# Performance work log

Measured on AMD Instinct MI355X. Metric: run time of the kernel, lower is better.

Reference implementation:

```python
import jax, jax.numpy as jnp
import numpy as np

K = 9          # neighbors (module default k=9, dilation=1 -> plain top-k)
COUT = 256     # out_channels
BN_EPS = 1e-5


def setup_inputs() -> dict:
    key = jax.random.key(0)
    k1, k2 = jax.random.split(key, 2)
    x = jax.random.normal(k1, (8, 128, 2048, 1), jnp.float32)          # [B,C,N,1]
    W = jax.random.normal(k2, (COUT, 2 * 128), jnp.float32) * 0.05     # 1x1 conv weight [Cout, 2C]
    gamma = jnp.ones((COUT,), jnp.float32)                             # BN affine scale
    beta = jnp.zeros((COUT,), jnp.float32)                             # BN affine shift
    return {"x": x, "W": W, "gamma": gamma, "beta": beta}


def reference(x, W, gamma, beta):
    # x: [B, C, N, 1] channels-first point features
    xt = jnp.transpose(x[..., 0], (0, 2, 1))                           # [B, N, C]
    B, N, C = xt.shape

    # --- dense KNN graph (matrix form): squared euclidean distance, k nearest ---
    sq = jnp.sum(xt * xt, axis=-1)                                     # [B, N]
    dist = sq[:, :, None] - 2.0 * jnp.einsum('bnc,bmc->bnm', xt, xt) + sq[:, None, :]
    _, nn_idx = jax.lax.top_k(-dist, K)                                # [B, N, K] neighbor indices

    # --- EdgeConv gather: x_i = center, x_j = neighbor ---
    x_j = jax.vmap(lambda f, i: f[i])(xt, nn_idx)                      # [B, N, K, C]
    x_i = xt[:, :, None, :]                                            # [B, N, 1, C]
    feat = jnp.concatenate(
        [jnp.broadcast_to(x_i, (B, N, K, C)), x_j - x_i], axis=-1)     # [B, N, K, 2C]

    # --- 1x1 conv (no bias) as GEMM over channel dim ---
    h = jnp.einsum('bnkc,oc->bnko', feat, W)                           # [B, N, K, Cout]

    # --- BatchNorm2d (training-mode batch stats over B,N,K per channel) ---
    mean = jnp.mean(h, axis=(0, 1, 2))
    var = jnp.var(h, axis=(0, 1, 2))
    hn = (h - mean) * jax.lax.rsqrt(var + BN_EPS) * gamma + beta

    # --- ReLU then max over k neighbors ---
    out = jnp.max(jax.nn.relu(hn), axis=2)                             # [B, N, Cout]
    return jnp.transpose(out, (0, 2, 1))                               # [B, Cout, N]
```

## Files before the change

### kernel.cpp

```cpp
#include <hip/hip_runtime.h>
#include <float.h>
#include <math.h>

#define BATCH 8
#define CHN   128
#define NPTS  2048
#define KNN   9
#define NOUT  256
#define TOTCNT (BATCH*NPTS*KNN)

typedef __attribute__((ext_vector_type(8))) short short8;
typedef __attribute__((ext_vector_type(4))) float f32x4;

__device__ __forceinline__ unsigned short f2bf(float f) {
    unsigned int u = __float_as_uint(f);
    unsigned int r = (u + 0x7FFFu + ((u >> 16) & 1u)) >> 16;
    return (unsigned short)r;
}
__device__ __forceinline__ float bf2f(unsigned short h) {
    return __uint_as_float(((unsigned int)h) << 16);
}

__global__ __launch_bounds__(256) void prep_kernel(const float* __restrict__ x,
                                                   unsigned short* __restrict__ xhi,
                                                   unsigned short* __restrict__ xlo,
                                                   float* __restrict__ sqh) {
    __shared__ float xt[128 * 65];
    __shared__ float psq[256];
    const int b = blockIdx.x, n0 = blockIdx.y * 64, tid = threadIdx.x;
#pragma unroll 4
    for (int p = 0; p < 32; ++p) {
        int c = p * 4 + (tid >> 6), n = tid & 63;
        xt[c * 65 + n] = x[((size_t)b * CHN + c) * NPTS + n0 + n];
    }
    __syncthreads();
    const int n = tid >> 2, cq = tid & 3;
    size_t row = (size_t)(b * NPTS + n0 + n) * CHN;
    float s = 0.f;
#pragma unroll 8
    for (int j = 0; j < 32; ++j) {
        int c = cq * 32 + j;
        float f = xt[c * 65 + n];
        unsigned short h = f2bf(f);
        float hf = bf2f(h);
        unsigned short l = f2bf(f - hf);
        xhi[row + c] = h;
        xlo[row + c] = l;
        s += f * f;
    }
    psq[tid] = s;
    __syncthreads();
    if (tid < 64)
        sqh[b * NPTS + n0 + tid] =
            0.5f * (psq[tid*4] + psq[tid*4+1] + psq[tid*4+2] + psq[tid*4+3]);
}

__global__ __launch_bounds__(256) void wprep_kernel(const float* __restrict__ W,
                                                    unsigned short* __restrict__ whi,
                                                    unsigned short* __restrict__ wlo) {
    int t = blockIdx.x * 256 + threadIdx.x;
    int r = t >> 5, c0 = (t & 31) * 4;
#pragma unroll
    for (int e = 0; e < 4; ++e) {
        int c = c0 + e;
        float v = (r < 256) ? (W[r * 256 + c] - W[r * 256 + 128 + c])
                            : W[(r - 256) * 256 + 128 + c];
        unsigned short h = f2bf(v);
        float hf = bf2f(h);
        unsigned short l = f2bf(v - hf);
        whi[r * 128 + c] = h;
        wlo[r * 128 + c] = l;
    }
}

__global__ __launch_bounds__(256) void knn_mfma(const unsigned short* __restrict__ xhi,
                                                const unsigned short* __restrict__ xlo,
                                                const float* __restrict__ sqh,
                                                float* __restrict__ pd,
                                                int* __restrict__ pi) {
    __shared__ __align__(16) float dts[64 * 132];

    const int tid = threadIdx.x;
    const int b = blockIdx.x, q0 = blockIdx.y * 64, ms = blockIdx.z;
    const int msbase = ms * 512;
    const int wv = tid >> 6, lane = tid & 63;
    const int quad = lane >> 4, col = lane & 15;
    const int koff = quad * 8;
    const int mcol0 = wv * 32;
    const size_t xb = (size_t)b * NPTS * CHN;

    float dl[KNN]; int il[KNN];
#pragma unroll
    for (int k = 0; k < KNN; ++k) { dl[k] = FLT_MAX; il[k] = 0; }

    const int qsc = tid >> 2, ss = tid & 3;
    const int cb = ss * 32;

    auto ins = [&](float v, int idx) {
        if (v < dl[KNN - 1]) {
            bool c0b = v < dl[0];
#pragma unroll
            for (int k = KNN - 1; k >= 1; --k) {
                bool sh   = v < dl[k - 1];
                bool here = v < dl[k];
                float nd = sh ? dl[k - 1] : (here ? v : dl[k]);
                int   ni = sh ? il[k - 1] : (here ? idx : il[k]);
                dl[k] = nd; il[k] = ni;
            }
            if (c0b) { dl[0] = v; il[0] = idx; }
        }
    };

    for (int iter = 0; iter < 4; ++iter) {
        const int mbase = msbase + iter * 128;
        float sm[2];
#pragma unroll
        for (int j = 0; j < 2; ++j)
            sm[j] = sqh[b * NPTS + mbase + mcol0 + j * 16 + col];

        f32x4 acc[4][2];
#pragma unroll
        for (int i = 0; i < 4; ++i)
#pragma unroll
            for (int j = 0; j < 2; ++j) acc[i][j] = (f32x4)0.f;

        for (int chk = 0; chk < 4; ++chk) {
            short8 ah[4], al[4];
#pragma unroll
            for (int i = 0; i < 4; ++i) {
                size_t g = xb + (size_t)(q0 + i * 16 + col) * CHN + chk * 32 + koff;
                ah[i] = *(const short8*)&xhi[g];
                al[i] = *(const short8*)&xlo[g];
            }
#pragma unroll
            for (int j = 0; j < 2; ++j) {
                size_t g = xb + (size_t)(mbase + mcol0 + j * 16 + col) * CHN + chk * 32 + koff;
                short8 bh = *(const short8*)&xhi[g];
                short8 bl = *(const short8*)&xlo[g];
#pragma unroll
                for (int i = 0; i < 4; ++i) {
                    acc[i][j] = __builtin_amdgcn_mfma_f32_16x16x32_bf16(ah[i], bh, acc[i][j], 0, 0, 0);
                    acc[i][j] = __builtin_amdgcn_mfma_f32_16x16x32_bf16(ah[i], bl, acc[i][j], 0, 0, 0);
                    acc[i][j] = __builtin_amdgcn_mfma_f32_16x16x32_bf16(al[i], bh, acc[i][j], 0, 0, 0);
                }
            }
        }

        __syncthreads();
#pragma unroll
        for (int j = 0; j < 2; ++j)
#pragma unroll
            for (int i = 0; i < 4; ++i)
#pragma unroll
                for (int r = 0; r < 4; ++r) {
                    int q_ = i * 16 + quad * 4 + r;
                    dts[q_ * 132 + mcol0 + j * 16 + col] = sm[j] - acc[i][j][r];
                }
        __syncthreads();
        const int ibase = mbase + cb;
#pragma unroll
        for (int jj = 0; jj < 8; ++jj) {
            float4 v = *(const float4*)&dts[qsc * 132 + cb + jj * 4];
            float mn4 = fminf(fminf(v.x, v.y), fminf(v.z, v.w));
            if (mn4 < dl[KNN - 1]) {
                int ib = ibase + jj * 4;
                ins(v.x, ib); ins(v.y, ib + 1); ins(v.z, ib + 2); ins(v.w, ib + 3);
            }
        }
    }

    __syncthreads();
    float* md = dts;
    int*   mi = (int*)(dts + 2304);
#pragma unroll
    for (int k = 0; k < KNN; ++k) {
        md[qsc * 36 + ss * 9 + k] = dl[k];
        mi[qsc * 36 + ss * 9 + k] = il[k];
    }
    __syncthreads();
    if (tid < 64) {
        int base = tid * 36;
        int p0 = 0, p1 = 0, p2 = 0, p3 = 0;
        size_t ob = ((size_t)(b * NPTS + q0 + tid) * 4 + ms) * KNN;
        for (int k = 0; k < KNN; ++k) {
            float v0 = (p0 < KNN) ? md[base + p0]      : FLT_MAX;
            float v1 = (p1 < KNN) ? md[base + 9 + p1]  : FLT_MAX;
            float v2 = (p2 < KNN) ? md[base + 18 + p2] : FLT_MAX;
            float v3 = (p3 < KNN) ? md[base + 27 + p3] : FLT_MAX;
            float best = v0; int sel = 0;
            if (v1 < best) { best = v1; sel = 1; }
            if (v2 < best) { best = v2; sel = 2; }
            if (v3 < best) { best = v3; sel = 3; }
            int idx;
            if      (sel == 0) { idx = mi[base + p0];      p0++; }
            else if (sel == 1) { idx = mi[base + 9 + p1];  p1++; }
            else if (sel == 2) { idx = mi[base + 18 + p2]; p2++; }
            else               { idx = mi[base + 27 + p3]; p3++; }
            pd[ob + k] = best;
            pi[ob + k] = idx;
        }
    }
}

__global__ __launch_bounds__(256) void pq_mfma(const unsigned short* __restrict__ xhi,
                                               const unsigned short* __restrict__ xlo,
                                               const unsigned short* __restrict__ whi,
                                               const unsigned short* __restrict__ wlo,
                                               float* __restrict__ p,
                                               float* __restrict__ q) {
    const int tid = threadIdx.x;
    const int b = blockIdx.x, nt = blockIdx.y, ot = blockIdx.z;
    const int wv = tid >> 6, lane = tid & 63;
    const int quad = lane >> 4, col = lane & 15;
    const int koff = quad * 8;
    const size_t xb = (size_t)b * NPTS * CHN;
    const int nbase = nt * 256 + wv * 64;
    const int obase = ot * 64;

    f32x4 acc[4][4];
#pragma unroll
    for (int i = 0; i < 4; ++i)
#pragma unroll
        for (int j = 0; j < 4; ++j) acc[i][j] = (f32x4)0.f;

    for (int chk = 0; chk < 4; ++chk) {
        short8 ah[4], al[4];
#pragma unroll
        for (int i = 0; i < 4; ++i) {
            size_t g = xb + (size_t)(nbase + i * 16 + col) * CHN + chk * 32 + koff;
            ah[i] = *(const short8*)&xhi[g];
            al[i] = *(const short8*)&xlo[g];
        }
#pragma unroll
        for (int j = 0; j < 4; ++j) {
            size_t g = (size_t)(obase + j * 16 + col) * CHN + chk * 32 + koff;
            short8 bh = *(const short8*)&whi[g];
            short8 bl = *(const short8*)&wlo[g];
#pragma unroll
            for (int i = 0; i < 4; ++i) {
                acc[i][j] = __builtin_amdgcn_mfma_f32_16x16x32_bf16(ah[i], bh, acc[i][j], 0, 0, 0);
                acc[i][j] = __builtin_amdgcn_mfma_f32_16x16x32_bf16(ah[i], bl, acc[i][j], 0, 0, 0);
                acc[i][j] = __builtin_amdgcn_mfma_f32_16x16x32_bf16(al[i], bh, acc[i][j], 0, 0, 0);
            }
        }
    }
    float* dst = (ot < 4) ? p : q;
#pragma unroll
    for (int i = 0; i < 4; ++i)
#pragma unroll
        for (int j = 0; j < 4; ++j) {
            int oc = (obase + j * 16 + col) & 255;
#pragma unroll
            for (int r = 0; r < 4; ++r) {
                int n = nbase + i * 16 + quad * 4 + r;
                dst[(size_t)(b * NPTS + n) * NOUT + oc] = acc[i][j][r];
            }
        }
}

__global__ __launch_bounds__(256) void stats2_kernel(float* __restrict__ p,
                                                     const float* __restrict__ q,
                                                     const float* __restrict__ pd,
                                                     const int* __restrict__ pi,
                                                     float* __restrict__ stats,
                                                     float* __restrict__ hmn) {
    __shared__ int idx_s[32 * KNN];
    const int b = blockIdx.x, n0 = blockIdx.y * 32;
    const int o = threadIdx.x;
    if (threadIdx.x < 32) {
        size_t g = (size_t)(b * NPTS + n0 + threadIdx.x) * 36;
        const float* d = pd + g;
        const int*   i = pi + g;
        int p0 = 0, p1 = 0, p2 = 0, p3 = 0;
#pragma unroll
        for (int k = 0; k < KNN; ++k) {
            float v0 = (p0 < KNN) ? d[p0]      : FLT_MAX;
            float v1 = (p1 < KNN) ? d[9 + p1]  : FLT_MAX;
            float v2 = (p2 < KNN) ? d[18 + p2] : FLT_MAX;
            float v3 = (p3 < KNN) ? d[27 + p3] : FLT_MAX;
            float best = v0; int sel = 0;
            if (v1 < best) { best = v1; sel = 1; }
            if (v2 < best) { best = v2; sel = 2; }
            if (v3 < best) { best = v3; sel = 3; }
            int idx;
            if      (sel == 0) { idx = i[p0];      p0++; }
            else if (sel == 1) { idx = i[9 + p1];  p1++; }
            else if (sel == 2) { idx = i[18 + p2]; p2++; }
            else               { idx = i[27 + p3]; p3++; }
            idx_s[threadIdx.x * KNN + k] = idx;
        }
    }
    __syncthreads();
    const float* qb = q + (size_t)b * NPTS * NOUT + o;
    float s = 0.f, ss = 0.f;
    for (int qq = 0; qq < 32; ++qq) {
        size_t off = (size_t)(b * NPTS + n0 + qq) * NOUT + o;
        float pv = p[off];
        float h[KNN];
#pragma unroll
        for (int k = 0; k < KNN; ++k)
            h[k] = pv + qb[(size_t)idx_s[qq * KNN + k] * NOUT];
        float mx = h[0], mn = h[0];
#pragma unroll
        for (int k = 0; k < KNN; ++k) {
            s += h[k]; ss += h[k] * h[k];
            mx = fmaxf(mx, h[k]); mn = fminf(mn, h[k]);
        }
        p[off] = mx;
        hmn[off] = mn;
    }
    atomicAdd(&stats[o], s);
    atomicAdd(&stats[NOUT + o], ss);
}

__global__ __launch_bounds__(256) void final_kernel(const float* __restrict__ hmx,
                                                    const float* __restrict__ hmn,
                                                    const float* __restrict__ stats,
                                                    const float* __restrict__ gamma,
                                                    const float* __restrict__ beta,
                                                    float* __restrict__ out) {
    __shared__ float tr[256 * 17];
    const int b = blockIdx.x, n0 = blockIdx.y * 16;
    const int o = threadIdx.x;
    const float inv = 1.f / (float)TOTCNT;
    float mean = stats[o] * inv;
    float var  = stats[NOUT + o] * inv - mean * mean;
    float g    = gamma[o] / sqrtf(var + 1e-5f);
    float bet  = beta[o];
    const float* src = (g >= 0.f) ? hmx : hmn;
    for (int qq = 0; qq < 16; ++qq) {
        size_t off = (size_t)(b * NPTS + n0 + qq) * NOUT + o;
        float hn = (src[off] - mean) * g + bet;
        tr[o * 17 + qq] = fmaxf(hn, 0.f);
    }
    __syncthreads();
    int oo = threadIdx.x >> 4, qq = threadIdx.x & 15;
    for (int pass = 0; pass < 16; ++pass) {
        int o_ = pass * 16 + oo;
        out[((size_t)b * NOUT + o_) * NPTS + n0 + qq] = tr[o_ * 17 + qq];
    }
}

extern "C" void kernel_launch(void* const* d_in, const int* in_sizes, int n_in,
                              void* d_out, int out_size, void* d_ws, size_t ws_size,
                              hipStream_t stream) {
    (void)in_sizes; (void)n_in; (void)out_size; (void)ws_size;
    const float* x     = (const float*)d_in[0];
    const float* W     = (const float*)d_in[1];
    const float* gamma = (const float*)d_in[2];
    const float* beta  = (const float*)d_in[3];
    float* out = (float*)d_out;

    char* ws = (char*)d_ws;
    float*          p     = (float*)ws;
    float*          q     = (float*)(ws + (16u << 20));
    unsigned short* xhi   = (unsigned short*)(ws + (32u << 20));
    unsigned short* xlo   = (unsigned short*)(ws + (36u << 20));
    unsigned short* whi   = (unsigned short*)(ws + (40u << 20));
    unsigned short* wlo   = (unsigned short*)(ws + (40u << 20) + 131072);
    float*          hmn   = (float*)(ws + (32u << 20));
    float*          pd    = (float*)(ws + (48u << 20));
    int*            pi    = (int*)  (ws + (51u << 20));
    float*          sqh   = (float*)(ws + (54u << 20));
    float*          stats = (float*)(ws + (54u << 20) + 65536);

    hipMemsetAsync(stats, 0, 2 * NOUT * sizeof(float), stream);
    wprep_kernel <<<64,             256, 0, stream>>>(W, whi, wlo);
    prep_kernel  <<<dim3(8, 32),    256, 0, stream>>>(x, xhi, xlo, sqh);
    knn_mfma     <<<dim3(8, 32, 4), 256, 0, stream>>>(xhi, xlo, sqh, pd, pi);
    pq_mfma      <<<dim3(8, 8, 8),  256, 0, stream>>>(xhi, xlo, whi, wlo, p, q);
    stats2_kernel<<<dim3(8, 64),    256, 0, stream>>>(p, q, pd, pi, stats, hmn);
    final_kernel <<<dim3(8, 128),   256, 0, stream>>>(p, hmn, stats, gamma, beta, out);
}
```

Before: 220.5 us.

## Fuse stats and BN-final via cooperative grid sync, store q and min/max as bf16

Folds the weight-prep kernel into prep_kernel as an extra block row. It also merges the gather/stats and normalize/output kernels into one cooperative kernel. Per-point max/min stay in shared memory across a grid-wide sync, so they are no longer written to and re-read from global memory. The q projection and the max/min values are stored as bf16 to halve gather traffic. This trades away some precision, and the cooperative launch requires all 512 blocks to be co-resident.

```diff
diff --git a/kernel.cpp b/kernel.cpp
--- a/kernel.cpp
+++ b/kernel.cpp
@@ -1,6 +1,9 @@
 #include <hip/hip_runtime.h>
+#include <hip/hip_cooperative_groups.h>
 #include <float.h>
 #include <math.h>
+
+namespace cg = cooperative_groups;
 
 #define BATCH 8
 #define CHN   128
@@ -22,12 +25,30 @@
 }
 
 __global__ __launch_bounds__(256) void prep_kernel(const float* __restrict__ x,
+                                                   const float* __restrict__ W,
                                                    unsigned short* __restrict__ xhi,
                                                    unsigned short* __restrict__ xlo,
+                                                   unsigned short* __restrict__ whi,
+                                                   unsigned short* __restrict__ wlo,
                                                    float* __restrict__ sqh) {
     __shared__ float xt[128 * 65];
     __shared__ float psq[256];
-    const int b = blockIdx.x, n0 = blockIdx.y * 64, tid = threadIdx.x;
+    const int b = blockIdx.x, tid = threadIdx.x;
+    if (blockIdx.y == 32) {
+#pragma unroll
+        for (int e = 0; e < 32; ++e) {
+            int idx = e * 256 + tid;
+            int r = b * 64 + (idx >> 7), c = idx & 127;
+            float v = (r < 256) ? (W[r * 256 + c] - W[r * 256 + 128 + c])
+                                : W[(r - 256) * 256 + 128 + c];
+            unsigned short h = f2bf(v);
+            float hf = bf2f(h);
+            whi[r * 128 + c] = h;
+            wlo[r * 128 + c] = f2bf(v - hf);
+        }
+        return;
+    }
+    const int n0 = blockIdx.y * 64;
 #pragma unroll 4
     for (int p = 0; p < 32; ++p) {
         int c = p * 4 + (tid >> 6), n = tid & 63;
@@ -53,24 +74,6 @@
     if (tid < 64)
         sqh[b * NPTS + n0 + tid] =
             0.5f * (psq[tid*4] + psq[tid*4+1] + psq[tid*4+2] + psq[tid*4+3]);
-}
-
-__global__ __launch_bounds__(256) void wprep_kernel(const float* __restrict__ W,
-                                                    unsigned short* __restrict__ whi,
-                                                    unsigned short* __restrict__ wlo) {
-    int t = blockIdx.x * 256 + threadIdx.x;
-    int r = t >> 5, c0 = (t & 31) * 4;
-#pragma unroll
-    for (int e = 0; e < 4; ++e) {
-        int c = c0 + e;
-        float v = (r < 256) ? (W[r * 256 + c] - W[r * 256 + 128 + c])
-                            : W[(r - 256) * 256 + 128 + c];
-        unsigned short h = f2bf(v);
-        float hf = bf2f(h);
-        unsigned short l = f2bf(v - hf);
-        whi[r * 128 + c] = h;
-        wlo[r * 128 + c] = l;
-    }
 }
 
 __global__ __launch_bounds__(256) void knn_mfma(const unsigned short* __restrict__ xhi,
@@ -207,7 +210,7 @@
                                                const unsigned short* __restrict__ whi,
                                                const unsigned short* __restrict__ wlo,
                                                float* __restrict__ p,
-                                               float* __restrict__ q) {
+                                               unsigned short* __restrict__ q) {
     const int tid = threadIdx.x;
     const int b = blockIdx.x, nt = blockIdx.y, ot = blockIdx.z;
     const int wv = tid >> 6, lane = tid & 63;
@@ -244,7 +247,6 @@
             }
         }
     }
-    float* dst = (ot < 4) ? p : q;
 #pragma unroll
     for (int i = 0; i < 4; ++i)
 #pragma unroll
@@ -253,20 +255,28 @@
 #pragma unroll
             for (int r = 0; r < 4; ++r) {
                 int n = nbase + i * 16 + quad * 4 + r;
-                dst[(size_t)(b * NPTS + n) * NOUT + oc] = acc[i][j][r];
-            }
-        }
-}
-
-__global__ __launch_bounds__(256) void stats2_kernel(float* __restrict__ p,
-                                                     const float* __restrict__ q,
-                                                     const float* __restrict__ pd,
-                                                     const int* __restrict__ pi,
-                                                     float* __restrict__ stats,
-                                                     float* __restrict__ hmn) {
-    __shared__ int idx_s[32 * KNN];
+                size_t off = (size_t)(b * NPTS + n) * NOUT + oc;
+                if (ot < 4) p[off] = acc[i][j][r];
+                else        q[off] = f2bf(acc[i][j][r]);
+            }
+        }
+}
+
+__global__ __launch_bounds__(256) void fused_bn_kernel(const float* __restrict__ p,
+                                                       const unsigned short* __restrict__ qb,
+                                                       const float* __restrict__ pd,
+                                                       const int* __restrict__ pi,
+                                                       float* __restrict__ stats,
+                                                       const float* __restrict__ gamma,
+                                                       const float* __restrict__ beta,
+                                                       float* __restrict__ out) {
+    __shared__ unsigned short hmx_s[32 * 258];
+    __shared__ unsigned short hmn_s[32 * 258];
+    __shared__ int   idx_s[32 * KNN];
+    __shared__ float g_s[256], bet_s[256], mean_s[256];
     const int b = blockIdx.x, n0 = blockIdx.y * 32;
     const int o = threadIdx.x;
+
     if (threadIdx.x < 32) {
         size_t g = (size_t)(b * NPTS + n0 + threadIdx.x) * 36;
         const float* d = pd + g;
@@ -291,53 +301,45 @@
         }
     }
     __syncthreads();
-    const float* qb = q + (size_t)b * NPTS * NOUT + o;
+
+    const unsigned short* qbb = qb + (size_t)b * NPTS * NOUT + o;
     float s = 0.f, ss = 0.f;
     for (int qq = 0; qq < 32; ++qq) {
         size_t off = (size_t)(b * NPTS + n0 + qq) * NOUT + o;
         float pv = p[off];
-        float h[KNN];
-#pragma unroll
-        for (int k = 0; k < KNN; ++k)
-            h[k] = pv + qb[(size_t)idx_s[qq * KNN + k] * NOUT];
-        float mx = h[0], mn = h[0];
+        float mx = -FLT_MAX, mn = FLT_MAX;
 #pragma unroll
         for (int k = 0; k < KNN; ++k) {
-            s += h[k]; ss += h[k] * h[k];
-            mx = fmaxf(mx, h[k]); mn = fminf(mn, h[k]);
-        }
-        p[off] = mx;
-        hmn[off] = mn;
+            float h = pv + bf2f(qbb[(size_t)idx_s[qq * KNN + k] * NOUT]);
+            s += h; ss += h * h;
+            mx = fmaxf(mx, h); mn = fminf(mn, h);
+        }
+        hmx_s[qq * 258 + o] = f2bf(mx);
+        hmn_s[qq * 258 + o] = f2bf(mn);
     }
     atomicAdd(&stats[o], s);
     atomicAdd(&stats[NOUT + o], ss);
-}
-
-__global__ __launch_bounds__(256) void final_kernel(const float* __restrict__ hmx,
-                                                    const float* __restrict__ hmn,
-                                                    const float* __restrict__ stats,
-                                                    const float* __restrict__ gamma,
-                                                    const float* __restrict__ beta,
-                                                    float* __restrict__ out) {
-    __shared__ float tr[256 * 17];
-    const int b = blockIdx.x, n0 = blockIdx.y * 16;
-    const int o = threadIdx.x;
-    const float inv = 1.f / (float)TOTCNT;
-    float mean = stats[o] * inv;
-    float var  = stats[NOUT + o] * inv - mean * mean;
-    float g    = gamma[o] / sqrtf(var + 1e-5f);
-    float bet  = beta[o];
-    const float* src = (g >= 0.f) ? hmx : hmn;
-    for (int qq = 0; qq < 16; ++qq) {
-        size_t off = (size_t)(b * NPTS + n0 + qq) * NOUT + o;
-        float hn = (src[off] - mean) * g + bet;
-        tr[o * 17 + qq] = fmaxf(hn, 0.f);
-    }
-    __syncthreads();
-    int oo = threadIdx.x >> 4, qq = threadIdx.x & 15;
-    for (int pass = 0; pass < 16; ++pass) {
-        int o_ = pass * 16 + oo;
-        out[((size_t)b * NOUT + o_) * NPTS + n0 + qq] = tr[o_ * 17 + qq];
+    __threadfence();
+    cg::this_grid().sync();
+
+    {
+        const float inv = 1.f / (float)TOTCNT;
+        float mean = stats[o] * inv;
+        float var  = stats[NOUT + o] * inv - mean * mean;
+        g_s[o]    = gamma[o] / sqrtf(var + 1e-5f);
+        bet_s[o]  = beta[o];
+        mean_s[o] = mean;
+    }
+    __syncthreads();
+
+    const int qq2 = threadIdx.x & 31, og = threadIdx.x >> 5;
+#pragma unroll 4
+    for (int pass = 0; pass < 32; ++pass) {
+        int o_ = pass * 8 + og;
+        float g = g_s[o_];
+        float v = bf2f((g >= 0.f) ? hmx_s[qq2 * 258 + o_] : hmn_s[qq2 * 258 + o_]);
+        float hn = (v - mean_s[o_]) * g + bet_s[o_];
+        out[((size_t)b * NOUT + o_) * NPTS + n0 + qq2] = fmaxf(hn, 0.f);
     }
 }
 
@@ -353,22 +355,23 @@
 
     char* ws = (char*)d_ws;
     float*          p     = (float*)ws;
-    float*          q     = (float*)(ws + (16u << 20));
+    unsigned short* q     = (unsigned short*)(ws + (16u << 20));
     unsigned short* xhi   = (unsigned short*)(ws + (32u << 20));
     unsigned short* xlo   = (unsigned short*)(ws + (36u << 20));
     unsigned short* whi   = (unsigned short*)(ws + (40u << 20));
     unsigned short* wlo   = (unsigned short*)(ws + (40u << 20) + 131072);
-    float*          hmn   = (float*)(ws + (32u << 20));
     float*          pd    = (float*)(ws + (48u << 20));
     int*            pi    = (int*)  (ws + (51u << 20));
     float*          sqh   = (float*)(ws + (54u << 20));
     float*          stats = (float*)(ws + (54u << 20) + 65536);
 
     hipMemsetAsync(stats, 0, 2 * NOUT * sizeof(float), stream);
-    wprep_kernel <<<64,             256, 0, stream>>>(W, whi, wlo);
-    prep_kernel  <<<dim3(8, 32),    256, 0, stream>>>(x, xhi, xlo, sqh);
-    knn_mfma     <<<dim3(8, 32, 4), 256, 0, stream>>>(xhi, xlo, sqh, pd, pi);
-    pq_mfma      <<<dim3(8, 8, 8),  256, 0, stream>>>(xhi, xlo, whi, wlo, p, q);
-    stats2_kernel<<<dim3(8, 64),    256, 0, stream>>>(p, q, pd, pi, stats, hmn);
-    final_kernel <<<dim3(8, 128),   256, 0, stream>>>(p, hmn, stats, gamma, beta, out);
-}
+    prep_kernel<<<dim3(8, 33),    256, 0, stream>>>(x, W, xhi, xlo, whi, wlo, sqh);
+    knn_mfma   <<<dim3(8, 32, 4), 256, 0, stream>>>(xhi, xlo, sqh, pd, pi);
+    pq_mfma    <<<dim3(8, 8, 8),  256, 0, stream>>>(xhi, xlo, whi, wlo, p, q);
+
+    void* fargs[] = { (void*)&p, (void*)&q, (void*)&pd, (void*)&pi,
+                      (void*)&stats, (void*)&gamma, (void*)&beta, (void*)&out };
+    hipLaunchCooperativeKernel((void*)fused_bn_kernel, dim3(8, 64), dim3(256),
+                               fargs, 0, stream);
+}
```

Result: slower. 312.9 us (+41.9%).

## Merge weight prep into prep kernel and run KNN and PQ GEMM in one launch

Applied to the files above, without the earlier changes.

Weight hi/lo splitting now runs as an extra row of blocks inside the point prep kernel, and the KNN distance kernel and the P/Q projection GEMM become one launch that branches on blockIdx.z. This removes two launches and lets the two independent MFMA workloads share the GPU at the same time. Separately, the gather/stats kernel handles 16 points per block instead of 32, doubling its grid, and processes two points per iteration so more gathers are in flight. The costs are a divergent fused kernel whose branches differ in register and LDS needs, and twice as many atomic adds into the stats buffer.

```diff
diff --git a/kernel.cpp b/kernel.cpp
--- a/kernel.cpp
+++ b/kernel.cpp
@@ -22,12 +22,30 @@
 }
 
 __global__ __launch_bounds__(256) void prep_kernel(const float* __restrict__ x,
+                                                   const float* __restrict__ W,
                                                    unsigned short* __restrict__ xhi,
                                                    unsigned short* __restrict__ xlo,
+                                                   unsigned short* __restrict__ whi,
+                                                   unsigned short* __restrict__ wlo,
                                                    float* __restrict__ sqh) {
     __shared__ float xt[128 * 65];
     __shared__ float psq[256];
-    const int b = blockIdx.x, n0 = blockIdx.y * 64, tid = threadIdx.x;
+    const int b = blockIdx.x, tid = threadIdx.x;
+    if (blockIdx.y == 32) {
+#pragma unroll
+        for (int e = 0; e < 32; ++e) {
+            int idx = e * 256 + tid;
+            int r = b * 64 + (idx >> 7), c = idx & 127;
+            float v = (r < 256) ? (W[r * 256 + c] - W[r * 256 + 128 + c])
+                                : W[(r - 256) * 256 + 128 + c];
+            unsigned short h = f2bf(v);
+            float hf = bf2f(h);
+            whi[r * 128 + c] = h;
+            wlo[r * 128 + c] = f2bf(v - hf);
+        }
+        return;
+    }
+    const int n0 = blockIdx.y * 64;
 #pragma unroll 4
     for (int p = 0; p < 32; ++p) {
         int c = p * 4 + (tid >> 6), n = tid & 63;
@@ -55,39 +73,75 @@
             0.5f * (psq[tid*4] + psq[tid*4+1] + psq[tid*4+2] + psq[tid*4+3]);
 }
 
-__global__ __launch_bounds__(256) void wprep_kernel(const float* __restrict__ W,
-                                                    unsigned short* __restrict__ whi,
-                                                    unsigned short* __restrict__ wlo) {
-    int t = blockIdx.x * 256 + threadIdx.x;
-    int r = t >> 5, c0 = (t & 31) * 4;
-#pragma unroll
-    for (int e = 0; e < 4; ++e) {
-        int c = c0 + e;
-        float v = (r < 256) ? (W[r * 256 + c] - W[r * 256 + 128 + c])
-                            : W[(r - 256) * 256 + 128 + c];
-        unsigned short h = f2bf(v);
-        float hf = bf2f(h);
-        unsigned short l = f2bf(v - hf);
-        whi[r * 128 + c] = h;
-        wlo[r * 128 + c] = l;
-    }
-}
-
-__global__ __launch_bounds__(256) void knn_mfma(const unsigned short* __restrict__ xhi,
-                                                const unsigned short* __restrict__ xlo,
-                                                const float* __restrict__ sqh,
-                                                float* __restrict__ pd,
-                                                int* __restrict__ pi) {
+__global__ __launch_bounds__(256) void knnpq_mfma(const unsigned short* __restrict__ xhi,
+                                                  const unsigned short* __restrict__ xlo,
+                                                  const float* __restrict__ sqh,
+                                                  const unsigned short* __restrict__ whi,
+                                                  const unsigned short* __restrict__ wlo,
+                                                  float* __restrict__ pd,
+                                                  int* __restrict__ pi,
+                                                  float* __restrict__ p,
+                                                  float* __restrict__ q) {
     __shared__ __align__(16) float dts[64 * 132];
 
     const int tid = threadIdx.x;
-    const int b = blockIdx.x, q0 = blockIdx.y * 64, ms = blockIdx.z;
-    const int msbase = ms * 512;
+    const int b = blockIdx.x;
     const int wv = tid >> 6, lane = tid & 63;
     const int quad = lane >> 4, col = lane & 15;
     const int koff = quad * 8;
+    const size_t xb = (size_t)b * NPTS * CHN;
+
+    if (blockIdx.z >= 4) {
+        const int nt = blockIdx.y >> 2;
+        const int ot = ((blockIdx.y & 3) << 1) | (blockIdx.z - 4);
+        const int nbase = nt * 256 + wv * 64;
+        const int obase = ot * 64;
+
+        f32x4 acc[4][4];
+#pragma unroll
+        for (int i = 0; i < 4; ++i)
+#pragma unroll
+            for (int j = 0; j < 4; ++j) acc[i][j] = (f32x4)0.f;
+
+        for (int chk = 0; chk < 4; ++chk) {
+            short8 ah[4], al[4];
+#pragma unroll
+            for (int i = 0; i < 4; ++i) {
+                size_t g = xb + (size_t)(nbase + i * 16 + col) * CHN + chk * 32 + koff;
+                ah[i] = *(const short8*)&xhi[g];
+                al[i] = *(const short8*)&xlo[g];
+            }
+#pragma unroll
+            for (int j = 0; j < 4; ++j) {
+                size_t g = (size_t)(obase + j * 16 + col) * CHN + chk * 32 + koff;
+                short8 bh = *(const short8*)&whi[g];
+                short8 bl = *(const short8*)&wlo[g];
+#pragma unroll
+                for (int i = 0; i < 4; ++i) {
+                    acc[i][j] = __builtin_amdgcn_mfma_f32_16x16x32_bf16(ah[i], bh, acc[i][j], 0, 0, 0);
+                    acc[i][j] = __builtin_amdgcn_mfma_f32_16x16x32_bf16(ah[i], bl, acc[i][j], 0, 0, 0);
+                    acc[i][j] = __builtin_amdgcn_mfma_f32_16x16x32_bf16(al[i], bh, acc[i][j], 0, 0, 0);
+                }
+            }
+        }
+        float* dst = (ot < 4) ? p : q;
+#pragma unroll
+        for (int i = 0; i < 4; ++i)
+#pragma unroll
+            for (int j = 0; j < 4; ++j) {
+                int oc = (obase + j * 16 + col) & 255;
+#pragma unroll
+                for (int r = 0; r < 4; ++r) {
+                    int n = nbase + i * 16 + quad * 4 + r;
+                    dst[(size_t)(b * NPTS + n) * NOUT + oc] = acc[i][j][r];
+                }
+            }
+        return;
+    }
+
+    const int q0 = blockIdx.y * 64, ms = blockIdx.z;
+    const int msbase = ms * 512;
     const int mcol0 = wv * 32;
-    const size_t xb = (size_t)b * NPTS * CHN;
 
     float dl[KNN]; int il[KNN];
 #pragma unroll
@@ -202,72 +256,16 @@
     }
 }
 
-__global__ __launch_bounds__(256) void pq_mfma(const unsigned short* __restrict__ xhi,
-                                               const unsigned short* __restrict__ xlo,
-                                               const unsigned short* __restrict__ whi,
-                                               const unsigned short* __restrict__ wlo,
-                                               float* __restrict__ p,
-                                               float* __restrict__ q) {
-    const int tid = threadIdx.x;
-    const int b = blockIdx.x, nt = blockIdx.y, ot = blockIdx.z;
-    const int wv = tid >> 6, lane = tid & 63;
-    const int quad = lane >> 4, col = lane & 15;
-    const int koff = quad * 8;
-    const size_t xb = (size_t)b * NPTS * CHN;
-    const int nbase = nt * 256 + wv * 64;
-    const int obase = ot * 64;
-
-    f32x4 acc[4][4];
-#pragma unroll
-    for (int i = 0; i < 4; ++i)
-#pragma unroll
-        for (int j = 0; j < 4; ++j) acc[i][j] = (f32x4)0.f;
-
-    for (int chk = 0; chk < 4; ++chk) {
-        short8 ah[4], al[4];
-#pragma unroll
-        for (int i = 0; i < 4; ++i) {
-            size_t g = xb + (size_t)(nbase + i * 16 + col) * CHN + chk * 32 + koff;
-            ah[i] = *(const short8*)&xhi[g];
-            al[i] = *(const short8*)&xlo[g];
-        }
-#pragma unroll
-        for (int j = 0; j < 4; ++j) {
-            size_t g = (size_t)(obase + j * 16 + col) * CHN + chk * 32 + koff;
-            short8 bh = *(const short8*)&whi[g];
-            short8 bl = *(const short8*)&wlo[g];
-#pragma unroll
-            for (int i = 0; i < 4; ++i) {
-                acc[i][j] = __builtin_amdgcn_mfma_f32_16x16x32_bf16(ah[i], bh, acc[i][j], 0, 0, 0);
-                acc[i][j] = __builtin_amdgcn_mfma_f32_16x16x32_bf16(ah[i], bl, acc[i][j], 0, 0, 0);
-                acc[i][j] = __builtin_amdgcn_mfma_f32_16x16x32_bf16(al[i], bh, acc[i][j], 0, 0, 0);
-            }
-        }
-    }
-    float* dst = (ot < 4) ? p : q;
-#pragma unroll
-    for (int i = 0; i < 4; ++i)
-#pragma unroll
-        for (int j = 0; j < 4; ++j) {
-            int oc = (obase + j * 16 + col) & 255;
-#pragma unroll
-            for (int r = 0; r < 4; ++r) {
-                int n = nbase + i * 16 + quad * 4 + r;
-                dst[(size_t)(b * NPTS + n) * NOUT + oc] = acc[i][j][r];
-            }
-        }
-}
-
 __global__ __launch_bounds__(256) void stats2_kernel(float* __restrict__ p,
                                                      const float* __restrict__ q,
                                                      const float* __restrict__ pd,
                                                      const int* __restrict__ pi,
                                                      float* __restrict__ stats,
                                                      float* __restrict__ hmn) {
-    __shared__ int idx_s[32 * KNN];
-    const int b = blockIdx.x, n0 = blockIdx.y * 32;
+    __shared__ int idx_s[16 * KNN];
+    const int b = blockIdx.x, n0 = blockIdx.y * 16;
     const int o = threadIdx.x;
-    if (threadIdx.x < 32) {
+    if (threadIdx.x < 16) {
         size_t g = (size_t)(b * NPTS + n0 + threadIdx.x) * 36;
         const float* d = pd + g;
         const int*   i = pi + g;
@@ -293,21 +291,27 @@
     __syncthreads();
     const float* qb = q + (size_t)b * NPTS * NOUT + o;
     float s = 0.f, ss = 0.f;
-    for (int qq = 0; qq < 32; ++qq) {
-        size_t off = (size_t)(b * NPTS + n0 + qq) * NOUT + o;
-        float pv = p[off];
-        float h[KNN];
+    for (int qq = 0; qq < 16; qq += 2) {
+        size_t off0 = (size_t)(b * NPTS + n0 + qq) * NOUT + o;
+        size_t off1 = off0 + NOUT;
+        float pv0 = p[off0], pv1 = p[off1];
+        float h0[KNN], h1[KNN];
 #pragma unroll
         for (int k = 0; k < KNN; ++k)
-            h[k] = pv + qb[(size_t)idx_s[qq * KNN + k] * NOUT];
-        float mx = h[0], mn = h[0];
+            h0[k] = qb[(size_t)idx_s[qq * KNN + k] * NOUT];
+#pragma unroll
+        for (int k = 0; k < KNN; ++k)
+            h1[k] = qb[(size_t)idx_s[(qq + 1) * KNN + k] * NOUT];
+        float mx0 = -FLT_MAX, mn0 = FLT_MAX, mx1 = -FLT_MAX, mn1 = FLT_MAX;
 #pragma unroll
         for (int k = 0; k < KNN; ++k) {
-            s += h[k]; ss += h[k] * h[k];
-            mx = fmaxf(mx, h[k]); mn = fminf(mn, h[k]);
-        }
-        p[off] = mx;
-        hmn[off] = mn;
+            float a = pv0 + h0[k], c = pv1 + h1[k];
+            s += a + c; ss += a * a + c * c;
+            mx0 = fmaxf(mx0, a); mn0 = fminf(mn0, a);
+            mx1 = fmaxf(mx1, c); mn1 = fminf(mn1, c);
+        }
+        p[off0] = mx0; hmn[off0] = mn0;
+        p[off1] = mx1; hmn[off1] = mn1;
     }
     atomicAdd(&stats[o], s);
     atomicAdd(&stats[NOUT + o], ss);
@@ -365,10 +369,8 @@
     float*          stats = (float*)(ws + (54u << 20) + 65536);
 
     hipMemsetAsync(stats, 0, 2 * NOUT * sizeof(float), stream);
-    wprep_kernel <<<64,             256, 0, stream>>>(W, whi, wlo);
-    prep_kernel  <<<dim3(8, 32),    256, 0, stream>>>(x, xhi, xlo, sqh);
-    knn_mfma     <<<dim3(8, 32, 4), 256, 0, stream>>>(xhi, xlo, sqh, pd, pi);
-    pq_mfma      <<<dim3(8, 8, 8),  256, 0, stream>>>(xhi, xlo, whi, wlo, p, q);
-    stats2_kernel<<<dim3(8, 64),    256, 0, stream>>>(p, q, pd, pi, stats, hmn);
+    prep_kernel  <<<dim3(8, 33),    256, 0, stream>>>(x, W, xhi, xlo, whi, wlo, sqh);
+    knnpq_mfma   <<<dim3(8, 32, 6), 256, 0, stream>>>(xhi, xlo, sqh, whi, wlo, pd, pi, p, q);
+    stats2_kernel<<<dim3(8, 128),   256, 0, stream>>>(p, q, pd, pi, stats, hmn);
     final_kernel <<<dim3(8, 128),   256, 0, stream>>>(p, hmn, stats, gamma, beta, out);
 }
```

New measurement: 272.4 us. +23.5%, slower.
